# Performance work log

Measured on AMD Instinct MI355X. Metric: run time of the kernel, lower is better.

## Reference

```python
import jax, jax.numpy as jnp
import numpy as np

N_PAIRS = 1_600_000   # total neighbor pairs (len(idx_i))
N_ATOMS = 50_000      # number of distinct center atoms (avg 32 neighbors each)


def setup_inputs() -> dict:
    key = jax.random.key(0)
    # sorted center indices -> consecutive ragged segments, like a neighbor list
    idx_i = jnp.sort(jax.random.randint(key, (N_PAIRS,), 0, N_ATOMS, dtype=jnp.int32))
    return {"idx_i": idx_i}


def reference(idx_i):
    # NOTE: output shape is data-dependent (sum_i C(c_i,2)), so this runs eagerly
    # (the concrete sizes below are python ints pulled from the input values),
    # exactly mirroring torch.unique_consecutive + per-segment torch.combinations.
    n = idx_i.shape[0]
    # --- unique_consecutive(return_counts=True), vectorized ---
    change = jnp.concatenate([jnp.ones((1,), bool), idx_i[1:] != idx_i[:-1]])
    seg_id = jnp.cumsum(change.astype(jnp.int32)) - 1          # [n] segment id per pair
    n_seg = int(seg_id[-1]) + 1
    counts = jnp.bincount(seg_id, length=n_seg)                 # [n_seg] c_i
    seg_off = jnp.concatenate([jnp.zeros((1,), counts.dtype), jnp.cumsum(counts)[:-1]])
    # --- per-segment number of unordered pairs C(c,2) ---
    tri_counts = counts * (counts - 1) // 2
    tri_off = jnp.concatenate([jnp.zeros((1,), tri_counts.dtype), jnp.cumsum(tri_counts)[:-1]])
    T = int(jnp.sum(tri_counts))
    # --- one flat vectorized pass over all T triples ---
    idx_i_triples = jnp.repeat(jnp.arange(n_seg, dtype=jnp.int32), tri_counts,
                               total_repeat_length=T)           # [T] segment index
    r = jnp.arange(T, dtype=counts.dtype) - tri_off[idx_i_triples]  # local triple rank
    c = counts[idx_i_triples]                                   # segment size per triple
    M = c * (c - 1) // 2
    rr = M - 1 - r                                              # rank counted from the end
    # triangular-root decode of condensed upper-triangle index (c is small -> fp32 exact)
    a_rev = jnp.floor((jnp.sqrt(8.0 * rr.astype(jnp.float32) + 1.0) - 1.0) / 2.0).astype(c.dtype)
    a = c - 2 - a_rev                                           # first local neighbor pos
    b = c - 1 - (rr - a_rev * (a_rev + 1) // 2)                 # second local neighbor pos (> a)
    base = seg_off[idx_i_triples]
    idx_j_triples = base + a
    idx_k_triples = base + b
    return (idx_i_triples, idx_j_triples, idx_k_triples)
```

## Files before the change

kernel.cpp:

```cpp
#include <hip/hip_runtime.h>

#define THREADS 256

__device__ __forceinline__ int blockReduceSum(int v, int* sdata) {
    int tid = threadIdx.x;
    sdata[tid] = v;
    __syncthreads();
    for (int off = THREADS >> 1; off > 0; off >>= 1) {
        if (tid < off) sdata[tid] += sdata[tid + off];
        __syncthreads();
    }
    int r = sdata[0];
    __syncthreads();
    return r;
}

__device__ __forceinline__ int blockScanIncl(int v, int* sdata) {
    int tid = threadIdx.x;
    sdata[tid] = v;
    __syncthreads();
    for (int off = 1; off < THREADS; off <<= 1) {
        int t = 0;
        if (tid >= off) t = sdata[tid - off];
        __syncthreads();
        if (tid >= off) sdata[tid] += t;
        __syncthreads();
    }
    int r = sdata[tid];
    __syncthreads();
    return r;
}

__global__ void k_count(const int* __restrict__ idx, int n, int E,
                        int* __restrict__ chunkCnt) {
    __shared__ int sdata[THREADS];
    int base = (blockIdx.x * THREADS + threadIdx.x) * E;
    int cnt = 0;
    for (int j = 0; j < E; ++j) {
        int p = base + j;
        if (p < n) cnt += (p == 0) || (idx[p - 1] != idx[p]);
    }
    int tot = blockReduceSum(cnt, sdata);
    if (threadIdx.x == 0) chunkCnt[blockIdx.x] = tot;
}

__global__ void k_emit_starts(const int* __restrict__ idx, int n, int E, int NB,
                              const int* __restrict__ chunkCnt,
                              int* __restrict__ segOff,
                              int* __restrict__ nsegPtr) {
    __shared__ int sdata[THREADS];
    int tid = threadIdx.x;
    int c = blockIdx.x;

    int pv = 0;
    for (int i = tid; i < c; i += THREADS) pv += chunkCnt[i];
    int prefix = blockReduceSum(pv, sdata);

    int base = (c * THREADS + tid) * E;
    int cnt = 0;
    for (int j = 0; j < E; ++j) {
        int p = base + j;
        if (p < n) cnt += (p == 0) || (idx[p - 1] != idx[p]);
    }
    int incl = blockScanIncl(cnt, sdata);
    int off = prefix + incl - cnt;
    for (int j = 0; j < E; ++j) {
        int p = base + j;
        if (p < n && ((p == 0) || (idx[p - 1] != idx[p]))) segOff[off++] = p;
    }
    if (c == NB - 1 && tid == THREADS - 1) {
        int nseg = prefix + incl;
        *nsegPtr = nseg;
        segOff[nseg] = n;
    }
}

__global__ void k_tri_sums(const int* __restrict__ segOff,
                           const int* __restrict__ nsegPtr, int E,
                           int* __restrict__ triChunkSum) {
    __shared__ int sdata[THREADS];
    int nseg = *nsegPtr;
    int base = (blockIdx.x * THREADS + threadIdx.x) * E;
    int sum = 0;
    for (int j = 0; j < E; ++j) {
        int s = base + j;
        if (s < nseg) {
            int cc = segOff[s + 1] - segOff[s];
            sum += cc * (cc - 1) / 2;
        }
    }
    int tot = blockReduceSum(sum, sdata);
    if (threadIdx.x == 0) triChunkSum[blockIdx.x] = tot;
}

__global__ void k_emit_trioff(const int* __restrict__ segOff,
                              const int* __restrict__ nsegPtr, int E,
                              const int* __restrict__ triChunkSum,
                              int* __restrict__ triOff) {
    __shared__ int sdata[THREADS];
    int nseg = *nsegPtr;
    int tid = threadIdx.x;
    int c = blockIdx.x;

    int pv = 0;
    for (int i = tid; i < c; i += THREADS) pv += triChunkSum[i];
    int prefix = blockReduceSum(pv, sdata);

    int base = (c * THREADS + tid) * E;
    int cnt = 0;
    for (int j = 0; j < E; ++j) {
        int s = base + j;
        if (s < nseg) {
            int cc = segOff[s + 1] - segOff[s];
            cnt += cc * (cc - 1) / 2;
        }
    }
    int incl = blockScanIncl(cnt, sdata);
    int run = prefix + incl - cnt;
    for (int j = 0; j < E; ++j) {
        int s = base + j;
        if (s < nseg) {
            int cc = segOff[s + 1] - segOff[s];
            triOff[s] = run;
            run += cc * (cc - 1) / 2;
        }
    }
}

__global__ void k_fill(const int* __restrict__ segOff,
                       const int* __restrict__ triOff,
                       const int* __restrict__ nsegPtr,
                       int* __restrict__ outI, int* __restrict__ outJ,
                       int* __restrict__ outK) {
    int nseg = *nsegPtr;
    int wid = blockIdx.x * (THREADS / 64) + (threadIdx.x >> 6);
    int lane = threadIdx.x & 63;
    int nW = gridDim.x * (THREADS / 64);
    for (int s = wid; s < nseg; s += nW) {
        int baseP = segOff[s];
        int cc = segOff[s + 1] - baseP;
        int M = cc * (cc - 1) / 2;
        int t0 = triOff[s];
        for (int r = lane; r < M; r += 64) {
            int rr = M - 1 - r;
            int k = (int)floorf((sqrtf((float)(8 * rr + 1)) - 1.0f) * 0.5f);
            if (k < 0) k = 0;
            while ((k + 1) * (k + 2) / 2 <= rr) ++k;
            while (k * (k + 1) / 2 > rr) --k;
            int a = cc - 2 - k;
            int b = cc - 1 - (rr - k * (k + 1) / 2);
            int t = t0 + r;
            outI[t] = s;
            outJ[t] = baseP + a;
            outK[t] = baseP + b;
        }
    }
}

extern "C" void kernel_launch(void* const* d_in, const int* in_sizes, int n_in,
                              void* d_out, int out_size, void* d_ws, size_t ws_size,
                              hipStream_t stream) {
    const int* idx = (const int*)d_in[0];
    int n = in_sizes[0];
    int T = out_size / 3;
    int* out = (int*)d_out;
    int* ws = (int*)d_ws;

    int* nsegPtr     = ws;
    int* chunkCnt    = ws + 16;
    int* triChunkSum = ws + 16 + 1024;
    int* segOff      = ws + 16 + 2048;
    int* triOff      = segOff + (n + 1);

    int E = 8;
    while ((long long)(n + THREADS * E - 1) / (THREADS * E) > 1024) E <<= 1;
    int chunk = THREADS * E;
    int NB = (n + chunk - 1) / chunk;

    hipLaunchKernelGGL(k_count, dim3(NB), dim3(THREADS), 0, stream,
                       idx, n, E, chunkCnt);
    hipLaunchKernelGGL(k_emit_starts, dim3(NB), dim3(THREADS), 0, stream,
                       idx, n, E, NB, chunkCnt, segOff, nsegPtr);
    hipLaunchKernelGGL(k_tri_sums, dim3(NB), dim3(THREADS), 0, stream,
                       segOff, nsegPtr, E, triChunkSum);
    hipLaunchKernelGGL(k_emit_trioff, dim3(NB), dim3(THREADS), 0, stream,
                       segOff, nsegPtr, E, triChunkSum, triOff);
    hipLaunchKernelGGL(k_fill, dim3(4096), dim3(THREADS), 0, stream,
                       segOff, triOff, nsegPtr, out, out + T, out + 2 * T);
}
```

Before: 86.04 us.

## Merge triangle-offset scan into one kernel and emit paired int2 stores in fill

```diff
diff --git a/kernel.cpp b/kernel.cpp
--- a/kernel.cpp
+++ b/kernel.cpp
@@ -1,6 +1,8 @@
 #include <hip/hip_runtime.h>
 
 #define THREADS 256
+#define FILL_BLOCKS 4096
+#define TRIOFF_BLOCKS 64
 
 __device__ __forceinline__ int blockReduceSum(int v, int* sdata) {
     int tid = threadIdx.x;
@@ -49,14 +51,13 @@
                               int* __restrict__ segOff,
                               int* __restrict__ nsegPtr) {
     __shared__ int sdata[THREADS];
-    int tid = threadIdx.x;
-    int c = blockIdx.x;
+    int tid = threadIdx.x, bid = blockIdx.x;
 
     int pv = 0;
-    for (int i = tid; i < c; i += THREADS) pv += chunkCnt[i];
+    for (int i = tid; i < bid; i += THREADS) pv += chunkCnt[i];
     int prefix = blockReduceSum(pv, sdata);
 
-    int base = (c * THREADS + tid) * E;
+    int base = (bid * THREADS + tid) * E;
     int cnt = 0;
     for (int j = 0; j < E; ++j) {
         int p = base + j;
@@ -68,65 +69,48 @@
         int p = base + j;
         if (p < n && ((p == 0) || (idx[p - 1] != idx[p]))) segOff[off++] = p;
     }
-    if (c == NB - 1 && tid == THREADS - 1) {
+    if (bid == NB - 1 && tid == THREADS - 1) {
         int nseg = prefix + incl;
         *nsegPtr = nseg;
         segOff[nseg] = n;
     }
 }
 
-__global__ void k_tri_sums(const int* __restrict__ segOff,
-                           const int* __restrict__ nsegPtr, int E,
-                           int* __restrict__ triChunkSum) {
+__global__ void k_trioff(const int* __restrict__ segOff,
+                         const int* __restrict__ nsegPtr,
+                         int* __restrict__ triOff) {
     __shared__ int sdata[THREADS];
     int nseg = *nsegPtr;
-    int base = (blockIdx.x * THREADS + threadIdx.x) * E;
-    int sum = 0;
-    for (int j = 0; j < E; ++j) {
-        int s = base + j;
-        if (s < nseg) {
-            int cc = segOff[s + 1] - segOff[s];
-            sum += cc * (cc - 1) / 2;
-        }
-    }
-    int tot = blockReduceSum(sum, sdata);
-    if (threadIdx.x == 0) triChunkSum[blockIdx.x] = tot;
-}
-
-__global__ void k_emit_trioff(const int* __restrict__ segOff,
-                              const int* __restrict__ nsegPtr, int E,
-                              const int* __restrict__ triChunkSum,
-                              int* __restrict__ triOff) {
-    __shared__ int sdata[THREADS];
-    int nseg = *nsegPtr;
-    int tid = threadIdx.x;
-    int c = blockIdx.x;
+    int tid = threadIdx.x, bid = blockIdx.x;
+    int chunkSeg = (nseg + gridDim.x - 1) / gridDim.x;
+    int s0 = bid * chunkSeg; if (s0 > nseg) s0 = nseg;
+    int s1 = s0 + chunkSeg; if (s1 > nseg) s1 = nseg;
 
     int pv = 0;
-    for (int i = tid; i < c; i += THREADS) pv += triChunkSum[i];
+    for (int s = tid; s < s0; s += THREADS) {
+        int c = segOff[s + 1] - segOff[s];
+        pv += c * (c - 1) / 2;
+    }
     int prefix = blockReduceSum(pv, sdata);
 
-    int base = (c * THREADS + tid) * E;
-    int cnt = 0;
-    for (int j = 0; j < E; ++j) {
-        int s = base + j;
-        if (s < nseg) {
-            int cc = segOff[s + 1] - segOff[s];
-            cnt += cc * (cc - 1) / 2;
-        }
-    }
-    int incl = blockScanIncl(cnt, sdata);
-    int run = prefix + incl - cnt;
-    for (int j = 0; j < E; ++j) {
-        int s = base + j;
-        if (s < nseg) {
-            int cc = segOff[s + 1] - segOff[s];
-            triOff[s] = run;
-            run += cc * (cc - 1) / 2;
-        }
-    }
-}
-
+    int tE = (chunkSeg + THREADS - 1) / THREADS;
+    int a0 = s0 + tid * tE;
+    int a1 = a0 + tE; if (a1 > s1) a1 = s1;
+    int lsum = 0;
+    for (int s = a0; s < a1; ++s) {
+        int c = segOff[s + 1] - segOff[s];
+        lsum += c * (c - 1) / 2;
+    }
+    int incl = blockScanIncl(lsum, sdata);
+    int run = prefix + incl - lsum;
+    for (int s = a0; s < a1; ++s) {
+        int c = segOff[s + 1] - segOff[s];
+        triOff[s] = run;
+        run += c * (c - 1) / 2;
+    }
+}
+
+template <bool TEVEN>
 __global__ void k_fill(const int* __restrict__ segOff,
                        const int* __restrict__ triOff,
                        const int* __restrict__ nsegPtr,
@@ -138,21 +122,44 @@
     int nW = gridDim.x * (THREADS / 64);
     for (int s = wid; s < nseg; s += nW) {
         int baseP = segOff[s];
-        int cc = segOff[s + 1] - baseP;
-        int M = cc * (cc - 1) / 2;
+        int c = segOff[s + 1] - baseP;
+        int M = c * (c - 1) / 2;
+        if (M <= 0) continue;
         int t0 = triOff[s];
-        for (int r = lane; r < M; r += 64) {
-            int rr = M - 1 - r;
+        int h = t0 & 1;
+        if (h && lane == 0) {
+            outI[t0] = s;
+            outJ[t0] = baseP;
+            outK[t0] = baseP + 1;
+        }
+        int npairs = (M - h) >> 1;
+        for (int pi = lane; pi < npairs; pi += 64) {
+            int r0 = h + 2 * pi;
+            int rr = M - 1 - r0;
             int k = (int)floorf((sqrtf((float)(8 * rr + 1)) - 1.0f) * 0.5f);
             if (k < 0) k = 0;
             while ((k + 1) * (k + 2) / 2 <= rr) ++k;
             while (k * (k + 1) / 2 > rr) --k;
-            int a = cc - 2 - k;
-            int b = cc - 1 - (rr - k * (k + 1) / 2);
-            int t = t0 + r;
+            int a0v = c - 2 - k;
+            int b0v = c - 1 - (rr - k * (k + 1) / 2);
+            int a1v, b1v;
+            if (b0v == c - 1) { a1v = a0v + 1; b1v = a0v + 2; }
+            else              { a1v = a0v;     b1v = b0v + 1; }
+            int t = t0 + r0;
+            *reinterpret_cast<int2*>(outI + t) = make_int2(s, s);
+            *reinterpret_cast<int2*>(outK + t) = make_int2(baseP + b0v, baseP + b1v);
+            if (TEVEN) {
+                *reinterpret_cast<int2*>(outJ + t) = make_int2(baseP + a0v, baseP + a1v);
+            } else {
+                outJ[t]     = baseP + a0v;
+                outJ[t + 1] = baseP + a1v;
+            }
+        }
+        if (((M - h) & 1) && lane == 0) {
+            int t = t0 + M - 1;
             outI[t] = s;
-            outJ[t] = baseP + a;
-            outK[t] = baseP + b;
+            outJ[t] = baseP + c - 2;
+            outK[t] = baseP + c - 1;
         }
     }
 }
@@ -166,11 +173,10 @@
     int* out = (int*)d_out;
     int* ws = (int*)d_ws;
 
-    int* nsegPtr     = ws;
-    int* chunkCnt    = ws + 16;
-    int* triChunkSum = ws + 16 + 1024;
-    int* segOff      = ws + 16 + 2048;
-    int* triOff      = segOff + (n + 1);
+    int* nsegPtr  = ws;
+    int* chunkCnt = ws + 16;
+    int* segOff   = ws + 16 + 2048;
+    int* triOff   = segOff + (n + 1);
 
     int E = 8;
     while ((long long)(n + THREADS * E - 1) / (THREADS * E) > 1024) E <<= 1;
@@ -181,10 +187,15 @@
                        idx, n, E, chunkCnt);
     hipLaunchKernelGGL(k_emit_starts, dim3(NB), dim3(THREADS), 0, stream,
                        idx, n, E, NB, chunkCnt, segOff, nsegPtr);
-    hipLaunchKernelGGL(k_tri_sums, dim3(NB), dim3(THREADS), 0, stream,
-                       segOff, nsegPtr, E, triChunkSum);
-    hipLaunchKernelGGL(k_emit_trioff, dim3(NB), dim3(THREADS), 0, stream,
-                       segOff, nsegPtr, E, triChunkSum, triOff);
-    hipLaunchKernelGGL(k_fill, dim3(4096), dim3(THREADS), 0, stream,
-                       segOff, triOff, nsegPtr, out, out + T, out + 2 * T);
-}
+    hipLaunchKernelGGL(k_trioff, dim3(TRIOFF_BLOCKS), dim3(THREADS), 0, stream,
+                       segOff, nsegPtr, triOff);
+    if ((T & 1) == 0) {
+        hipLaunchKernelGGL((k_fill<true>), dim3(FILL_BLOCKS), dim3(THREADS), 0,
+                           stream, segOff, triOff, nsegPtr,
+                           out, out + T, out + 2 * T);
+    } else {
+        hipLaunchKernelGGL((k_fill<false>), dim3(FILL_BLOCKS), dim3(THREADS), 0,
+                           stream, segOff, triOff, nsegPtr,
+                           out, out + T, out + 2 * T);
+    }
+}
```

Result: slower. 103.8 us (+20.7%).
